# Kernel tuning notes

Hardware: AMD Instinct MI355X
Metric: run time of the kernel (lower is better)

The kernel has to match this reference:

```python
import jax, jax.numpy as jnp
import numpy as np

B, T, D = 64, 2048, 512

def setup_inputs() -> dict:
    key = jax.random.key(0)
    k1, k2, k3, k4 = jax.random.split(key, 4)
    query = jax.random.normal(k1, (B, D), dtype=jnp.float32)
    key_t = jax.random.normal(k2, (B, T, D), dtype=jnp.float32)
    value = jax.random.normal(k3, (B, T, D), dtype=jnp.float32)
    mask = jax.random.randint(k4, (B, T), 0, 2) == 1  # True = masked out
    return {"query": query, "key": key_t, "value": value, "mask": mask}

def reference(query, key, value, mask):
    # energy[b,t] = <key[b,t,:], query[b,:]>
    energy = jnp.einsum('btd,bd->bt', key, query)
    energy = jnp.where(mask, -jnp.inf, energy)
    attention = jax.nn.softmax(energy, axis=1)  # [B,T]
    context = jnp.einsum('bt,btd->bd', attention, value)  # [B,D]
    return (context, attention)
```

## Files before the change

### kernel.cpp

```cpp
#include <hip/hip_runtime.h>
#include <math.h>

#define BB 64
#define TT 2048
#define DD 512
#define TCH 16
#define TC (TT / TCH)

__global__ __launch_bounds__(256) void energy_kernel(
    const float* __restrict__ q, const float* __restrict__ k,
    const int* __restrict__ mask, float* __restrict__ energy) {
  const int wave = threadIdx.x >> 6;
  const int lane = threadIdx.x & 63;
  const long long row = (long long)blockIdx.x * 4 + wave;
  const int b = (int)(row >> 11);

  const float4* kp4 = (const float4*)(k + row * DD);
  const float4* qp4 = (const float4*)(q + (long long)b * DD);

  float4 ka = kp4[lane];
  float4 kb = kp4[lane + 64];
  float4 qa = qp4[lane];
  float4 qb = qp4[lane + 64];

  float s = ka.x * qa.x + ka.y * qa.y + ka.z * qa.z + ka.w * qa.w +
            kb.x * qb.x + kb.y * qb.y + kb.z * qb.z + kb.w * qb.w;

#pragma unroll
  for (int off = 32; off; off >>= 1) s += __shfl_down(s, off, 64);

  if (lane == 0) {
    energy[row] = mask[row] ? -INFINITY : s;
  }
}

__global__ __launch_bounds__(256) void softmax_kernel(
    const float* __restrict__ energy, float* __restrict__ attn) {
  const int b = blockIdx.x;
  const int tid = threadIdx.x;
  const int wave = tid >> 6;
  const int lane = tid & 63;

  float vals[8];
  float m = -INFINITY;
#pragma unroll
  for (int i = 0; i < 8; i++) {
    vals[i] = energy[b * TT + i * 256 + tid];
    m = fmaxf(m, vals[i]);
  }
#pragma unroll
  for (int off = 32; off; off >>= 1) m = fmaxf(m, __shfl_xor(m, off, 64));

  __shared__ float sm[4];
  __shared__ float ss[4];
  if (lane == 0) sm[wave] = m;
  __syncthreads();
  m = fmaxf(fmaxf(sm[0], sm[1]), fmaxf(sm[2], sm[3]));

  float ssum = 0.f;
#pragma unroll
  for (int i = 0; i < 8; i++) {
    vals[i] = __expf(vals[i] - m);
    ssum += vals[i];
  }
#pragma unroll
  for (int off = 32; off; off >>= 1) ssum += __shfl_xor(ssum, off, 64);
  if (lane == 0) ss[wave] = ssum;
  __syncthreads();
  ssum = ss[0] + ss[1] + ss[2] + ss[3];

  const float inv = 1.0f / ssum;
#pragma unroll
  for (int i = 0; i < 8; i++) {
    attn[b * TT + i * 256 + tid] = vals[i] * inv;
  }
}

__global__ __launch_bounds__(128) void pv_partial(
    const float* __restrict__ attn, const float* __restrict__ v,
    float* __restrict__ partial) {
  const int b = blockIdx.x;
  const int tc = blockIdx.y;
  const int tid = threadIdx.x;

  const float4* vp = (const float4*)(v + ((long long)b * TT + (long long)tc * TC) * DD);
  const float* ap = attn + b * TT + tc * TC;

  float4 acc = {0.f, 0.f, 0.f, 0.f};
#pragma unroll 4
  for (int t = 0; t < TC; t++) {
    const float a = ap[t];
    const float4 vv = vp[t * 128 + tid];
    acc.x += a * vv.x;
    acc.y += a * vv.y;
    acc.z += a * vv.z;
    acc.w += a * vv.w;
  }
  ((float4*)partial)[(b * TCH + tc) * 128 + tid] = acc;
}

__global__ __launch_bounds__(256) void pv_reduce(
    const float* __restrict__ partial, float* __restrict__ ctx) {
  const int i = blockIdx.x * 256 + threadIdx.x;
  const int b = i >> 9;
  const int d = i & 511;
  float s = 0.f;
#pragma unroll
  for (int tc = 0; tc < TCH; tc++) s += partial[((b * TCH + tc) << 9) + d];
  ctx[i] = s;
}

extern "C" void kernel_launch(void* const* d_in, const int* in_sizes, int n_in,
                              void* d_out, int out_size, void* d_ws, size_t ws_size,
                              hipStream_t stream) {
  const float* q    = (const float*)d_in[0];
  const float* k    = (const float*)d_in[1];
  const float* v    = (const float*)d_in[2];
  const int*   mask = (const int*)d_in[3];

  float* out  = (float*)d_out;
  float* ctx  = out;
  float* attn = out + BB * DD;

  float* energy  = (float*)d_ws;
  float* partial = energy + BB * TT;

  energy_kernel<<<BB * TT / 4, 256, 0, stream>>>(q, k, mask, energy);
  softmax_kernel<<<BB, 256, 0, stream>>>(energy, attn);
  pv_partial<<<dim3(BB, TCH), 128, 0, stream>>>(attn, v, partial);
  pv_reduce<<<BB * DD / 256, 256, 0, stream>>>(partial, ctx);
}
```

Baseline: 106.6 us.

## Fuse softmax, PV partial and reduction into one kernel with atomic tickets

Removes the separate softmax and reduce kernels. Each PV block recomputes the row softmax statistics from energy and computes its attention weights inline. The last block per batch, found through an atomic counter, sums the partials into the context output. TCH is doubled so more blocks are launched. The cost is redundant max/sum work and extra energy reads in every block, plus reliance on counters zeroed by the energy kernel and on threadfence ordering.

```diff
diff --git a/kernel.cpp b/kernel.cpp
--- a/kernel.cpp
+++ b/kernel.cpp
@@ -4,12 +4,15 @@
 #define BB 64
 #define TT 2048
 #define DD 512
-#define TCH 16
+#define TCH 32
 #define TC (TT / TCH)
 
 __global__ __launch_bounds__(256) void energy_kernel(
     const float* __restrict__ q, const float* __restrict__ k,
-    const int* __restrict__ mask, float* __restrict__ energy) {
+    const int* __restrict__ mask, float* __restrict__ energy,
+    unsigned int* __restrict__ counters) {
+  if (blockIdx.x == 0 && threadIdx.x < BB) counters[threadIdx.x] = 0u;
+
   const int wave = threadIdx.x >> 6;
   const int lane = threadIdx.x & 63;
   const long long row = (long long)blockIdx.x * 4 + wave;
@@ -34,80 +37,92 @@
   }
 }
 
-__global__ __launch_bounds__(256) void softmax_kernel(
-    const float* __restrict__ energy, float* __restrict__ attn) {
+__global__ __launch_bounds__(128) void pv_fused(
+    const float* __restrict__ energy, const float* __restrict__ v,
+    float* __restrict__ attn, float* __restrict__ ctx,
+    float* __restrict__ partial, unsigned int* __restrict__ counters) {
   const int b = blockIdx.x;
+  const int tc = blockIdx.y;
   const int tid = threadIdx.x;
   const int wave = tid >> 6;
   const int lane = tid & 63;
 
-  float vals[8];
+  __shared__ float sred[2];
+  __shared__ unsigned int sticket;
+
+  const float4* e4 = (const float4*)(energy + b * TT);
+  float4 ev[4];
   float m = -INFINITY;
 #pragma unroll
-  for (int i = 0; i < 8; i++) {
-    vals[i] = energy[b * TT + i * 256 + tid];
-    m = fmaxf(m, vals[i]);
+  for (int i = 0; i < 4; i++) {
+    ev[i] = e4[i * 128 + tid];
+    m = fmaxf(m, fmaxf(fmaxf(ev[i].x, ev[i].y), fmaxf(ev[i].z, ev[i].w)));
   }
 #pragma unroll
   for (int off = 32; off; off >>= 1) m = fmaxf(m, __shfl_xor(m, off, 64));
-
-  __shared__ float sm[4];
-  __shared__ float ss[4];
-  if (lane == 0) sm[wave] = m;
+  if (lane == 0) sred[wave] = m;
   __syncthreads();
-  m = fmaxf(fmaxf(sm[0], sm[1]), fmaxf(sm[2], sm[3]));
+  m = fmaxf(sred[0], sred[1]);
+  __syncthreads();
 
   float ssum = 0.f;
 #pragma unroll
-  for (int i = 0; i < 8; i++) {
-    vals[i] = __expf(vals[i] - m);
-    ssum += vals[i];
+  for (int i = 0; i < 4; i++) {
+    ev[i].x = __expf(ev[i].x - m);
+    ev[i].y = __expf(ev[i].y - m);
+    ev[i].z = __expf(ev[i].z - m);
+    ev[i].w = __expf(ev[i].w - m);
+    ssum += ev[i].x + ev[i].y + ev[i].z + ev[i].w;
   }
 #pragma unroll
   for (int off = 32; off; off >>= 1) ssum += __shfl_xor(ssum, off, 64);
-  if (lane == 0) ss[wave] = ssum;
+  if (lane == 0) sred[wave] = ssum;
   __syncthreads();
-  ssum = ss[0] + ss[1] + ss[2] + ss[3];
+  ssum = sred[0] + sred[1];
+  const float inv = 1.0f / ssum;
 
-  const float inv = 1.0f / ssum;
+  if (tc == 0) {
+    float4* a4 = (float4*)(attn + b * TT);
 #pragma unroll
-  for (int i = 0; i < 8; i++) {
-    attn[b * TT + i * 256 + tid] = vals[i] * inv;
+    for (int i = 0; i < 4; i++) {
+      float4 o;
+      o.x = ev[i].x * inv; o.y = ev[i].y * inv;
+      o.z = ev[i].z * inv; o.w = ev[i].w * inv;
+      a4[i * 128 + tid] = o;
+    }
   }
-}
 
-__global__ __launch_bounds__(128) void pv_partial(
-    const float* __restrict__ attn, const float* __restrict__ v,
-    float* __restrict__ partial) {
-  const int b = blockIdx.x;
-  const int tc = blockIdx.y;
-  const int tid = threadIdx.x;
-
+  const float* ep = energy + b * TT + tc * TC;
   const float4* vp = (const float4*)(v + ((long long)b * TT + (long long)tc * TC) * DD);
-  const float* ap = attn + b * TT + tc * TC;
 
   float4 acc = {0.f, 0.f, 0.f, 0.f};
-#pragma unroll 4
+#pragma unroll 8
   for (int t = 0; t < TC; t++) {
-    const float a = ap[t];
+    const float a = __expf(ep[t] - m) * inv;
     const float4 vv = vp[t * 128 + tid];
     acc.x += a * vv.x;
     acc.y += a * vv.y;
     acc.z += a * vv.z;
     acc.w += a * vv.w;
   }
-  ((float4*)partial)[(b * TCH + tc) * 128 + tid] = acc;
-}
 
-__global__ __launch_bounds__(256) void pv_reduce(
-    const float* __restrict__ partial, float* __restrict__ ctx) {
-  const int i = blockIdx.x * 256 + threadIdx.x;
-  const int b = i >> 9;
-  const int d = i & 511;
-  float s = 0.f;
+  float4* p4 = (float4*)partial;
+  p4[(b * TCH + tc) * 128 + tid] = acc;
+
+  __threadfence();
+  __syncthreads();
+  if (tid == 0) sticket = atomicAdd(&counters[b], 1u);
+  __syncthreads();
+  if (sticket == TCH - 1) {
+    __threadfence();
+    float4 s = {0.f, 0.f, 0.f, 0.f};
 #pragma unroll
-  for (int tc = 0; tc < TCH; tc++) s += partial[((b * TCH + tc) << 9) + d];
-  ctx[i] = s;
+    for (int j = 0; j < TCH; j++) {
+      const float4 pv = p4[(b * TCH + j) * 128 + tid];
+      s.x += pv.x; s.y += pv.y; s.z += pv.z; s.w += pv.w;
+    }
+    ((float4*)ctx)[b * 128 + tid] = s;
+  }
 }
 
 extern "C" void kernel_launch(void* const* d_in, const int* in_sizes, int n_in,
@@ -122,11 +137,10 @@
   float* ctx  = out;
   float* attn = out + BB * DD;
 
-  float* energy  = (float*)d_ws;
-  float* partial = energy + BB * TT;
+  float*        energy   = (float*)d_ws;
+  float*        partial  = energy + BB * TT;
+  unsigned int* counters = (unsigned int*)(partial + BB * TCH * DD);
 
-  energy_kernel<<<BB * TT / 4, 256, 0, stream>>>(q, k, mask, energy);
-  softmax_kernel<<<BB, 256, 0, stream>>>(energy, attn);
-  pv_partial<<<dim3(BB, TCH), 128, 0, stream>>>(attn, v, partial);
-  pv_reduce<<<BB * DD / 256, 256, 0, stream>>>(partial, ctx);
+  energy_kernel<<<BB * TT / 4, 256, 0, stream>>>(q, k, mask, energy, counters);
+  pv_fused<<<dim3(BB, TCH), 128, 0, stream>>>(energy, v, attn, ctx, partial, counters);
 }
```

Result: slower. 285.9 us (+168.1%).

## Fuse energy, chunk softmax and PV into split-T flash-decode kernel

Applied to the files above, without the earlier changes.

Replaces the four-kernel pipeline with a single fused kernel that, per (batch, 64-row chunk), computes the energies, a local max and exp-sum, and the weighted V partial sum. A second combine kernel rescales the partials and the attention weights using online-softmax statistics. This drops the energy round-trip and two kernel launches. In exchange it adds per-chunk rescaling and leaves only 2048 blocks of 256 threads for streaming K and V, which limits the memory parallelism.

```diff
diff --git a/kernel.cpp b/kernel.cpp
--- a/kernel.cpp
+++ b/kernel.cpp
@@ -4,110 +4,123 @@
 #define BB 64
 #define TT 2048
 #define DD 512
-#define TCH 16
+#define TCH 32
 #define TC (TT / TCH)
 
-__global__ __launch_bounds__(256) void energy_kernel(
+__global__ __launch_bounds__(256) void fused_chunk(
     const float* __restrict__ q, const float* __restrict__ k,
-    const int* __restrict__ mask, float* __restrict__ energy) {
-  const int wave = threadIdx.x >> 6;
-  const int lane = threadIdx.x & 63;
-  const long long row = (long long)blockIdx.x * 4 + wave;
-  const int b = (int)(row >> 11);
+    const float* __restrict__ v, const int* __restrict__ mask,
+    float* __restrict__ wbuf,
+    float* __restrict__ partial,
+    float* __restrict__ mstat,
+    float* __restrict__ sstat) {
+  const int b = blockIdx.x;
+  const int tc = blockIdx.y;
+  const int tid = threadIdx.x;
+  const int wave = tid >> 6;
+  const int lane = tid & 63;
 
-  const float4* kp4 = (const float4*)(k + row * DD);
-  const float4* qp4 = (const float4*)(q + (long long)b * DD);
+  __shared__ float se[TC];
+  __shared__ float sw[TC];
 
-  float4 ka = kp4[lane];
-  float4 kb = kp4[lane + 64];
-  float4 qa = qp4[lane];
-  float4 qb = qp4[lane + 64];
+  const int t0 = tc * TC;
+  const long long base = ((long long)b * TT + t0) * DD;
 
-  float s = ka.x * qa.x + ka.y * qa.y + ka.z * qa.z + ka.w * qa.w +
-            kb.x * qb.x + kb.y * qb.y + kb.z * qb.z + kb.w * qb.w;
+  const float4* qp4 = (const float4*)(q + b * DD);
+  const float4 qa = qp4[lane];
+  const float4 qb = qp4[lane + 64];
 
+#pragma unroll 2
+  for (int i = 0; i < TC / 4; ++i) {
+    const int r = wave * (TC / 4) + i;
+    const float4* kp4 = (const float4*)(k + base + (long long)r * DD);
+    const float4 ka = kp4[lane];
+    const float4 kb = kp4[lane + 64];
+    float s = ka.x * qa.x + ka.y * qa.y + ka.z * qa.z + ka.w * qa.w +
+              kb.x * qb.x + kb.y * qb.y + kb.z * qb.z + kb.w * qb.w;
 #pragma unroll
-  for (int off = 32; off; off >>= 1) s += __shfl_down(s, off, 64);
+    for (int off = 32; off; off >>= 1) s += __shfl_down(s, off, 64);
+    if (lane == 0) se[r] = s;
+  }
+  __syncthreads();
 
-  if (lane == 0) {
-    energy[row] = mask[row] ? -INFINITY : s;
+  if (wave == 0) {
+    const float e = mask[b * TT + t0 + lane] ? -INFINITY : se[lane];
+    float m = e;
+#pragma unroll
+    for (int off = 32; off; off >>= 1) m = fmaxf(m, __shfl_xor(m, off, 64));
+    const float msafe = (m == -INFINITY) ? 0.f : m;
+    const float w = __expf(e - msafe);
+    float ss = w;
+#pragma unroll
+    for (int off = 32; off; off >>= 1) ss += __shfl_xor(ss, off, 64);
+    sw[lane] = w;
+    wbuf[b * TT + t0 + lane] = w;
+    if (lane == 0) {
+      mstat[b * TCH + tc] = m;
+      sstat[b * TCH + tc] = ss;
+    }
   }
+  __syncthreads();
+
+  const float2* vp = (const float2*)(v + base);
+  float2 acc = {0.f, 0.f};
+#pragma unroll 8
+  for (int t = 0; t < TC; ++t) {
+    const float a = sw[t];
+    const float2 vv = vp[t * 256 + tid];
+    acc.x += a * vv.x;
+    acc.y += a * vv.y;
+  }
+  ((float2*)partial)[(b * TCH + tc) * 256 + tid] = acc;
 }
 
-__global__ __launch_bounds__(256) void softmax_kernel(
-    const float* __restrict__ energy, float* __restrict__ attn) {
+__global__ __launch_bounds__(256) void combine(
+    const float* __restrict__ wbuf, const float* __restrict__ partial,
+    const float* __restrict__ mstat, const float* __restrict__ sstat,
+    float* __restrict__ ctx, float* __restrict__ attn) {
   const int b = blockIdx.x;
   const int tid = threadIdx.x;
   const int wave = tid >> 6;
   const int lane = tid & 63;
 
-  float vals[8];
-  float m = -INFINITY;
+  __shared__ float scw[TCH];
+
+  if (wave == 0) {
+    const float m = (lane < TCH) ? mstat[b * TCH + lane] : -INFINITY;
+    float mb = m;
 #pragma unroll
-  for (int i = 0; i < 8; i++) {
-    vals[i] = energy[b * TT + i * 256 + tid];
-    m = fmaxf(m, vals[i]);
+    for (int off = 32; off; off >>= 1) mb = fmaxf(mb, __shfl_xor(mb, off, 64));
+    const float cw = (lane < TCH) ? __expf(m - mb) : 0.f;
+    float S = (lane < TCH) ? sstat[b * TCH + lane] * cw : 0.f;
+#pragma unroll
+    for (int off = 32; off; off >>= 1) S += __shfl_xor(S, off, 64);
+    if (lane < TCH) scw[lane] = cw / S;
   }
+  __syncthreads();
+
+  const float2* p2 = (const float2*)partial;
+  float2 a = {0.f, 0.f};
 #pragma unroll
-  for (int off = 32; off; off >>= 1) m = fmaxf(m, __shfl_xor(m, off, 64));
+  for (int c = 0; c < TCH; ++c) {
+    const float cwn = scw[c];
+    const float2 p = p2[(b * TCH + c) * 256 + tid];
+    a.x += cwn * p.x;
+    a.y += cwn * p.y;
+  }
+  ((float2*)ctx)[b * 256 + tid] = a;
 
-  __shared__ float sm[4];
-  __shared__ float ss[4];
-  if (lane == 0) sm[wave] = m;
-  __syncthreads();
-  m = fmaxf(fmaxf(sm[0], sm[1]), fmaxf(sm[2], sm[3]));
-
-  float ssum = 0.f;
+  const float4* w4 = (const float4*)(wbuf + b * TT);
+  float4* a4 = (float4*)(attn + b * TT);
 #pragma unroll
-  for (int i = 0; i < 8; i++) {
-    vals[i] = __expf(vals[i] - m);
-    ssum += vals[i];
+  for (int i = 0; i < 2; ++i) {
+    const int idx = i * 256 + tid;
+    const float cwn = scw[(idx * 4) >> 6];
+    const float4 w = w4[idx];
+    float4 o;
+    o.x = w.x * cwn; o.y = w.y * cwn; o.z = w.z * cwn; o.w = w.w * cwn;
+    a4[idx] = o;
   }
-#pragma unroll
-  for (int off = 32; off; off >>= 1) ssum += __shfl_xor(ssum, off, 64);
-  if (lane == 0) ss[wave] = ssum;
-  __syncthreads();
-  ssum = ss[0] + ss[1] + ss[2] + ss[3];
-
-  const float inv = 1.0f / ssum;
-#pragma unroll
-  for (int i = 0; i < 8; i++) {
-    attn[b * TT + i * 256 + tid] = vals[i] * inv;
-  }
-}
-
-__global__ __launch_bounds__(128) void pv_partial(
-    const float* __restrict__ attn, const float* __restrict__ v,
-    float* __restrict__ partial) {
-  const int b = blockIdx.x;
-  const int tc = blockIdx.y;
-  const int tid = threadIdx.x;
-
-  const float4* vp = (const float4*)(v + ((long long)b * TT + (long long)tc * TC) * DD);
-  const float* ap = attn + b * TT + tc * TC;
-
-  float4 acc = {0.f, 0.f, 0.f, 0.f};
-#pragma unroll 4
-  for (int t = 0; t < TC; t++) {
-    const float a = ap[t];
-    const float4 vv = vp[t * 128 + tid];
-    acc.x += a * vv.x;
-    acc.y += a * vv.y;
-    acc.z += a * vv.z;
-    acc.w += a * vv.w;
-  }
-  ((float4*)partial)[(b * TCH + tc) * 128 + tid] = acc;
-}
-
-__global__ __launch_bounds__(256) void pv_reduce(
-    const float* __restrict__ partial, float* __restrict__ ctx) {
-  const int i = blockIdx.x * 256 + threadIdx.x;
-  const int b = i >> 9;
-  const int d = i & 511;
-  float s = 0.f;
-#pragma unroll
-  for (int tc = 0; tc < TCH; tc++) s += partial[((b * TCH + tc) << 9) + d];
-  ctx[i] = s;
 }
 
 extern "C" void kernel_launch(void* const* d_in, const int* in_sizes, int n_in,
@@ -122,11 +135,12 @@
   float* ctx  = out;
   float* attn = out + BB * DD;
 
-  float* energy  = (float*)d_ws;
-  float* partial = energy + BB * TT;
+  float* wbuf    = (float*)d_ws;
+  float* partial = wbuf + BB * TT;
+  float* mstat   = partial + BB * TCH * DD;
+  float* sstat   = mstat + BB * TCH;
 
-  energy_kernel<<<BB * TT / 4, 256, 0, stream>>>(q, k, mask, energy);
-  softmax_kernel<<<BB, 256, 0, stream>>>(energy, attn);
-  pv_partial<<<dim3(BB, TCH), 128, 0, stream>>>(attn, v, partial);
-  pv_reduce<<<BB * DD / 256, 256, 0, stream>>>(partial, ctx);
+  fused_chunk<<<dim3(BB, TCH), 256, 0, stream>>>(q, k, v, mask, wbuf, partial,
+                                                 mstat, sstat);
+  combine<<<BB, 256, 0, stream>>>(wbuf, partial, mstat, sstat, ctx, attn);
 }
```

After: 120.6 us. +13.1%, slower.

## Fuse softmax into PV pass using atomic per-batch max and deferred normalization

Applied to the files above, without the earlier changes.

The energy kernel now also computes a per-block max and publishes it through an order-preserving unsigned atomicMax per batch row, so the separate softmax kernel is removed. The PV kernel computes unnormalized exp weights into shared memory, writes them out along with per-chunk sums, and accumulates partial context. A finalize kernel reduces the chunk sums, scales both context and attention by the reciprocal, and replaces the old reduce kernel. This drops one launch and one round trip of the attention row, but adds a memset, per-block atomics, and an extra weight buffer write and read.

```diff
diff --git a/kernel.cpp b/kernel.cpp
--- a/kernel.cpp
+++ b/kernel.cpp
@@ -4,16 +4,27 @@
 #define BB 64
 #define TT 2048
 #define DD 512
-#define TCH 16
-#define TC (TT / TCH)
+#define NCH 16
+#define TC (TT / NCH)
+
+__device__ __forceinline__ unsigned fenc(float f) {
+  unsigned b = __float_as_uint(f);
+  return (b & 0x80000000u) ? ~b : (b | 0x80000000u);
+}
+__device__ __forceinline__ float fdec(unsigned u) {
+  return __uint_as_float((u & 0x80000000u) ? (u & 0x7FFFFFFFu) : ~u);
+}
 
 __global__ __launch_bounds__(256) void energy_kernel(
     const float* __restrict__ q, const float* __restrict__ k,
-    const int* __restrict__ mask, float* __restrict__ energy) {
+    const int* __restrict__ mask, float* __restrict__ energy,
+    unsigned* __restrict__ mslot) {
   const int wave = threadIdx.x >> 6;
   const int lane = threadIdx.x & 63;
   const long long row = (long long)blockIdx.x * 4 + wave;
   const int b = (int)(row >> 11);
+
+  __shared__ float smax[4];
 
   const float4* kp4 = (const float4*)(k + row * DD);
   const float4* qp4 = (const float4*)(q + (long long)b * DD);
@@ -30,84 +41,104 @@
   for (int off = 32; off; off >>= 1) s += __shfl_down(s, off, 64);
 
   if (lane == 0) {
-    energy[row] = mask[row] ? -INFINITY : s;
+    const float e = mask[row] ? -INFINITY : s;
+    energy[row] = e;
+    smax[wave] = e;
+  }
+  __syncthreads();
+  if (threadIdx.x == 0) {
+    const float mb = fmaxf(fmaxf(smax[0], smax[1]), fmaxf(smax[2], smax[3]));
+    atomicMax(&mslot[b], fenc(mb));
   }
 }
 
-__global__ __launch_bounds__(256) void softmax_kernel(
-    const float* __restrict__ energy, float* __restrict__ attn) {
+__global__ __launch_bounds__(128) void pv_slim(
+    const float* __restrict__ energy, const float* __restrict__ v,
+    const unsigned* __restrict__ mslot,
+    float* __restrict__ wbuf, float* __restrict__ partial,
+    float* __restrict__ sstat) {
   const int b = blockIdx.x;
+  const int c = blockIdx.y;
   const int tid = threadIdx.x;
   const int wave = tid >> 6;
   const int lane = tid & 63;
 
-  float vals[8];
-  float m = -INFINITY;
+  __shared__ float sa[TC];
+  __shared__ float sws[2];
+
+  const unsigned mu = mslot[b];
+  const float m = (mu == 0u) ? 0.f : fdec(mu);
+
+  const float e = energy[b * TT + c * TC + tid];
+  const float w = __expf(e - m);
+  sa[tid] = w;
+  wbuf[b * TT + c * TC + tid] = w;
+
+  float ws_ = w;
 #pragma unroll
-  for (int i = 0; i < 8; i++) {
-    vals[i] = energy[b * TT + i * 256 + tid];
-    m = fmaxf(m, vals[i]);
-  }
-#pragma unroll
-  for (int off = 32; off; off >>= 1) m = fmaxf(m, __shfl_xor(m, off, 64));
+  for (int off = 32; off; off >>= 1) ws_ += __shfl_xor(ws_, off, 64);
+  if (lane == 0) sws[wave] = ws_;
+  __syncthreads();
+  if (tid == 0) sstat[b * NCH + c] = sws[0] + sws[1];
 
-  __shared__ float sm[4];
-  __shared__ float ss[4];
-  if (lane == 0) sm[wave] = m;
-  __syncthreads();
-  m = fmaxf(fmaxf(sm[0], sm[1]), fmaxf(sm[2], sm[3]));
-
-  float ssum = 0.f;
-#pragma unroll
-  for (int i = 0; i < 8; i++) {
-    vals[i] = __expf(vals[i] - m);
-    ssum += vals[i];
-  }
-#pragma unroll
-  for (int off = 32; off; off >>= 1) ssum += __shfl_xor(ssum, off, 64);
-  if (lane == 0) ss[wave] = ssum;
-  __syncthreads();
-  ssum = ss[0] + ss[1] + ss[2] + ss[3];
-
-  const float inv = 1.0f / ssum;
-#pragma unroll
-  for (int i = 0; i < 8; i++) {
-    attn[b * TT + i * 256 + tid] = vals[i] * inv;
-  }
-}
-
-__global__ __launch_bounds__(128) void pv_partial(
-    const float* __restrict__ attn, const float* __restrict__ v,
-    float* __restrict__ partial) {
-  const int b = blockIdx.x;
-  const int tc = blockIdx.y;
-  const int tid = threadIdx.x;
-
-  const float4* vp = (const float4*)(v + ((long long)b * TT + (long long)tc * TC) * DD);
-  const float* ap = attn + b * TT + tc * TC;
-
+  const float4* vp = (const float4*)(v + ((long long)b * TT + c * TC) * DD);
   float4 acc = {0.f, 0.f, 0.f, 0.f};
-#pragma unroll 4
+#pragma unroll 8
   for (int t = 0; t < TC; t++) {
-    const float a = ap[t];
+    const float a = sa[t];
     const float4 vv = vp[t * 128 + tid];
     acc.x += a * vv.x;
     acc.y += a * vv.y;
     acc.z += a * vv.z;
     acc.w += a * vv.w;
   }
-  ((float4*)partial)[(b * TCH + tc) * 128 + tid] = acc;
+  ((float4*)partial)[(b * NCH + c) * 128 + tid] = acc;
 }
 
-__global__ __launch_bounds__(256) void pv_reduce(
-    const float* __restrict__ partial, float* __restrict__ ctx) {
-  const int i = blockIdx.x * 256 + threadIdx.x;
-  const int b = i >> 9;
-  const int d = i & 511;
-  float s = 0.f;
+__global__ __launch_bounds__(256) void finalize(
+    const float* __restrict__ wbuf, const float* __restrict__ partial,
+    const float* __restrict__ sstat,
+    float* __restrict__ ctx, float* __restrict__ attn) {
+  const int b = blockIdx.x;
+  const int tid = threadIdx.x;
+  const int lane = tid & 63;
+
+  __shared__ float sinv;
+
+  if (tid < 64) {
+    float s = (lane < NCH) ? sstat[b * NCH + lane] : 0.f;
+    s += __shfl_xor(s, 8, 64);
+    s += __shfl_xor(s, 4, 64);
+    s += __shfl_xor(s, 2, 64);
+    s += __shfl_xor(s, 1, 64);
+    if (lane == 0) sinv = 1.0f / s;
+  }
+  __syncthreads();
+  const float inv = sinv;
+
+  const float2* p2 = (const float2*)partial;
+  float2 a = {0.f, 0.f};
 #pragma unroll
-  for (int tc = 0; tc < TCH; tc++) s += partial[((b * TCH + tc) << 9) + d];
-  ctx[i] = s;
+  for (int c = 0; c < NCH; c++) {
+    const float2 p = p2[(b * NCH + c) * 256 + tid];
+    a.x += p.x;
+    a.y += p.y;
+  }
+  float2 o;
+  o.x = a.x * inv;
+  o.y = a.y * inv;
+  ((float2*)ctx)[b * 256 + tid] = o;
+
+  const float4* w4 = (const float4*)(wbuf + b * TT);
+  float4* a4 = (float4*)(attn + b * TT);
+#pragma unroll
+  for (int i = 0; i < 2; i++) {
+    const int idx = i * 256 + tid;
+    const float4 w = w4[idx];
+    float4 ao;
+    ao.x = w.x * inv; ao.y = w.y * inv; ao.z = w.z * inv; ao.w = w.w * inv;
+    a4[idx] = ao;
+  }
 }
 
 extern "C" void kernel_launch(void* const* d_in, const int* in_sizes, int n_in,
@@ -122,11 +153,14 @@
   float* ctx  = out;
   float* attn = out + BB * DD;
 
-  float* energy  = (float*)d_ws;
-  float* partial = energy + BB * TT;
+  float*    energy  = (float*)d_ws;
+  float*    wbuf    = energy + BB * TT;
+  float*    partial = wbuf + BB * TT;
+  float*    sstat   = partial + BB * NCH * DD;
+  unsigned* mslot   = (unsigned*)(sstat + BB * NCH);
 
-  energy_kernel<<<BB * TT / 4, 256, 0, stream>>>(q, k, mask, energy);
-  softmax_kernel<<<BB, 256, 0, stream>>>(energy, attn);
-  pv_partial<<<dim3(BB, TCH), 128, 0, stream>>>(attn, v, partial);
-  pv_reduce<<<BB * DD / 256, 256, 0, stream>>>(partial, ctx);
+  hipMemsetAsync(mslot, 0, BB * sizeof(unsigned), stream);
+  energy_kernel<<<BB * TT / 4, 256, 0, stream>>>(q, k, mask, energy, mslot);
+  pv_slim<<<dim3(BB, NCH), 128, 0, stream>>>(energy, v, mslot, wbuf, partial, sstat);
+  finalize<<<BB, 256, 0, stream>>>(wbuf, partial, sstat, ctx, attn);
 }
```

New measurement: 283.2 us. +165.5%, slower.
